# Kernel optimization log

Hardware: AMD Instinct MI355X
Metric: run time of the kernel (lower is better)

The kernel has to match this reference:

```python
import jax, jax.numpy as jnp
import numpy as np

LATENT, HID, STYLE, S = 16, 256, 64, 10
B = 16384

def _lin_init(key, fan_in, shape):
    # torch nn.Linear default: U(-1/sqrt(fan_in), 1/sqrt(fan_in))
    bound = 1.0 / np.sqrt(fan_in)
    return jax.random.uniform(key, shape, jnp.float32, -bound, bound)

def setup_inputs() -> dict:
    key = jax.random.key(0)
    ks = jax.random.split(key, 32)
    inp = {
        "z": jax.random.normal(ks[0], (B, LATENT), jnp.float32),
        "y": jax.random.randint(ks[1], (B,), 0, S),
        # shared 4-layer MLP
        "sw0": _lin_init(ks[2], LATENT, (LATENT, HID)), "sb0": _lin_init(ks[3], LATENT, (HID,)),
        "sw1": _lin_init(ks[4], HID, (HID, HID)), "sb1": _lin_init(ks[5], HID, (HID,)),
        "sw2": _lin_init(ks[6], HID, (HID, HID)), "sb2": _lin_init(ks[7], HID, (HID,)),
        "sw3": _lin_init(ks[8], HID, (HID, HID)), "sb3": _lin_init(ks[9], HID, (HID,)),
        # unshared per-speaker branches, stacked over speaker axis
        "uw0": _lin_init(ks[10], HID, (S, HID, HID)), "ub0": _lin_init(ks[11], HID, (S, HID)),
        "uw1": _lin_init(ks[12], HID, (S, HID, HID)), "ub1": _lin_init(ks[13], HID, (S, HID)),
        "uw2": _lin_init(ks[14], HID, (S, HID, HID)), "ub2": _lin_init(ks[15], HID, (S, HID)),
        "uw3": _lin_init(ks[16], HID, (S, HID, STYLE)), "ub3": _lin_init(ks[17], HID, (S, STYLE)),
    }
    return inp

def reference(z, y, sw0, sb0, sw1, sb1, sw2, sb2, sw3, sb3,
              uw0, ub0, uw1, ub1, uw2, ub2, uw3, ub3):
    relu = jax.nn.relu
    # shared trunk: [B, HID]
    h = relu(z @ sw0 + sb0)
    h = relu(h @ sw1 + sb1)
    h = relu(h @ sw2 + sb2)
    h = relu(h @ sw3 + sb3)
    # all speaker branches computed for every sample (faithful to original)
    t = relu(jnp.einsum('bh,shk->bsk', h, uw0) + ub0)  # [B, S, HID]
    t = relu(jnp.einsum('bsh,shk->bsk', t, uw1) + ub1)
    t = relu(jnp.einsum('bsh,shk->bsk', t, uw2) + ub2)
    out = jnp.einsum('bsh,shk->bsk', t, uw3) + ub3      # [B, S, STYLE]
    # gather branch by speaker id
    s = out[jnp.arange(out.shape[0]), y]                # [B, STYLE]
    return s
```

## Files before the change

### kernel.cpp

```cpp
#include <hip/hip_runtime.h>

#define B_TOT 16384
#define LAT   16
#define HID   256
#define STY   64
#define NS    10
#define RB    16
#define RB64  64
#define PAD   20
#define NBK   64

#define WS_CNT   0
#define WS_SEG   16
#define WS_BLK   32
#define WS_BCNT  64
#define WS_IDX   (WS_BCNT + NBK*NS)
#define IDX_CAP  (B_TOT + NS*RB64)
#define WS_INTS  (WS_IDX + IDX_CAP)
#define WGT_OFF_EL (((WS_INTS*4 + 255)/256)*128 + 384)
#define TOT_WEL  2334720
#define N_CHUNK  4560

typedef __attribute__((ext_vector_type(8))) short bf16x8;
typedef __attribute__((ext_vector_type(4))) float f32x4;

static __device__ __forceinline__ ushort f2bf(float x) {
    union { float f; unsigned u; } c; c.f = x;
    unsigned u = c.u;
    unsigned r = u + 0x7FFFu + ((u >> 16) & 1u);
    return (ushort)(r >> 16);
}

__global__ __launch_bounds__(256) void k_blkhist(const int* __restrict__ y, int* __restrict__ ws) {
    __shared__ int h[NS];
    int t = threadIdx.x;
    if (t < NS) h[t] = 0;
    __syncthreads();
    atomicAdd(&h[y[blockIdx.x * 256 + t]], 1);
    __syncthreads();
    if (t < NS) ws[WS_BCNT + blockIdx.x * NS + t] = h[t];
}

__global__ __launch_bounds__(256) void k_prep2(const int* __restrict__ y, int* __restrict__ ws, int rb) {
    __shared__ int tot_sh[NS], excl_sh[NS], off_sh[NS];
    const int t = threadIdx.x, wv = t >> 6, l = t & 63;
    const int myb = blockIdx.x;

    for (int s = wv; s < NS; s += 4) {
        int c = ws[WS_BCNT + l * NS + s];
        int inc = c;
        #pragma unroll
        for (int o = 1; o < 64; o <<= 1) {
            int v = __shfl_up(inc, o, 64);
            if (l >= o) inc += v;
        }
        int tot = __shfl(inc, 63, 64);
        int exc = __shfl(inc, myb, 64) - __shfl(c, myb, 64);
        if (l == 0) { tot_sh[s] = tot; excl_sh[s] = exc; }
    }
    __syncthreads();
    if (t < NS) {
        int ab = 0, ae = 0;
        for (int q = 0; q < t; ++q) {
            int cq = tot_sh[q];
            int nb = (cq + rb - 1) / rb;
            ab += nb; ae += nb * rb;
        }
        off_sh[t] = ae + excl_sh[t];
        if (myb == 0) {
            ws[WS_CNT + t] = tot_sh[t];
            ws[WS_SEG + t] = ae;
            ws[WS_BLK + t] = ab;
        }
    }
    if (myb == 0 && t == 0) {
        int ab = 0;
        for (int q = 0; q < NS; ++q) ab += (tot_sh[q] + rb - 1) / rb;
        ws[WS_BLK + NS] = ab;
    }
    __syncthreads();
    int b = myb * 256 + t;
    int p = atomicAdd(&off_sh[y[b]], 1);
    ws[WS_IDX + p] = b;
}

__global__ __launch_bounds__(256) void k_conv(
    const float* __restrict__ sw0, const float* __restrict__ sw1,
    const float* __restrict__ sw2, const float* __restrict__ sw3,
    const float* __restrict__ uw0, const float* __restrict__ uw1,
    const float* __restrict__ uw2, const float* __restrict__ uw3,
    ushort* __restrict__ wgt,
    const int* __restrict__ y, int* __restrict__ ws)
{
    __shared__ float tile[4][32][18];
    __shared__ int h[NS];

    if (blockIdx.x < NBK) {
        int t = threadIdx.x;
        if (t < NS) h[t] = 0;
        __syncthreads();
        atomicAdd(&h[y[blockIdx.x * 256 + t]], 1);
        __syncthreads();
        if (t < NS) ws[WS_BCNT + blockIdx.x * NS + t] = h[t];
    }

    int wid = blockIdx.x * 4 + (threadIdx.x >> 6);
    int wv  = threadIdx.x >> 6;
    int l   = threadIdx.x & 63;
    int lc  = l & 15, lh = l >> 4;

    const float* src; int Ksrc, N, kb, nt;
    if (wid < 16) {
        src = sw0; Ksrc = LAT; N = 256; kb = 0; nt = wid;
    } else if (wid < 400) {
        int c = wid - 16; int ly = c >> 7; int r = c & 127;
        src = (ly == 0 ? sw1 : ly == 1 ? sw2 : sw3);
        Ksrc = 256; N = 256; kb = r >> 4; nt = r & 15;
    } else {
        int c = wid - 400; int s = c / 416; int r = c % 416;
        if (r < 384) {
            int ly = r >> 7; int rr = r & 127;
            src = (ly == 0 ? uw0 : ly == 1 ? uw1 : uw2) + (long)s * 65536;
            Ksrc = 256; N = 256; kb = rr >> 4; nt = rr & 15;
        } else {
            int rr = r - 384;
            src = uw3 + (long)s * 16384;
            Ksrc = 256; N = STY; kb = rr >> 2; nt = rr & 3;
        }
    }

    #pragma unroll
    for (int it = 0; it < 2; ++it) {
        int r = it * 16 + (l >> 2);
        int k = kb * 32 + r;
        float4 v = make_float4(0.f, 0.f, 0.f, 0.f);
        if (k < Ksrc) v = *(const float4*)(src + (long)k * N + nt * 16 + (l & 3) * 4);
        int c = (l & 3) * 4;
        tile[wv][r][c] = v.x; tile[wv][r][c + 1] = v.y;
        tile[wv][r][c + 2] = v.z; tile[wv][r][c + 3] = v.w;
    }
    __syncthreads();

    ushort v[8];
    #pragma unroll
    for (int j = 0; j < 8; ++j) v[j] = f2bf(tile[wv][lh * 8 + j][lc]);
    uint4 o;
    o.x = (unsigned)v[0] | ((unsigned)v[1] << 16);
    o.y = (unsigned)v[2] | ((unsigned)v[3] << 16);
    o.z = (unsigned)v[4] | ((unsigned)v[5] << 16);
    o.w = (unsigned)v[6] | ((unsigned)v[7] << 16);
    *(uint4*)(wgt + (long)wid * 512 + l * 8) = o;
}

__global__ __launch_bounds__(512, 4) void k_main_bf(
    const float* __restrict__ z, const int* __restrict__ ws,
    const ushort* __restrict__ wgt,
    const float* __restrict__ sb0, const float* __restrict__ sb1,
    const float* __restrict__ sb2, const float* __restrict__ sb3,
    const float* __restrict__ ub0, const float* __restrict__ ub1,
    const float* __restrict__ ub2, const float* __restrict__ ub3,
    float* __restrict__ out)
{
    int bid = blockIdx.x;
    {
        int nwg = gridDim.x, q8 = nwg >> 3, r8 = nwg & 7;
        int x = bid & 7, p = bid >> 3;
        bid = (x < r8 ? x * (q8 + 1) : r8 * (q8 + 1) + (x - r8) * q8) + p;
    }
    if (bid >= ws[WS_BLK + NS]) return;

    int s = 0;
    #pragma unroll
    for (int q = 0; q < NS - 1; ++q)
        if (bid >= ws[WS_BLK + q + 1]) s = q + 1;
    const int loc  = bid - ws[WS_BLK + s];
    int nval = ws[WS_CNT + s] - loc * RB64;
    if (nval > RB64) nval = RB64;
    const int base = ws[WS_SEG + s] + loc * RB64;

    __shared__ ushort act[2][32][64][8];

    const int t = threadIdx.x, w = t >> 6, l = t & 63;
    const int lc = l & 15, lh = l >> 4;
    const int nt0 = w * 2;

    if (t < 256) {
        int row = t >> 2, q = t & 3;
        int gb  = ws[WS_IDX + base + row];
        if (row >= nval) gb = 0;
        float4 zv = *(const float4*)(z + (long)gb * LAT + q * 4);
        ushort4 pv; pv.x = f2bf(zv.x); pv.y = f2bf(zv.y); pv.z = f2bf(zv.z); pv.w = f2bf(zv.w);
        *(ushort4*)&act[0][q >> 1][row][(q & 1) * 4] = pv;
        ushort4 zr; zr.x = zr.y = zr.z = zr.w = 0;
        *(ushort4*)&act[0][2 + (q >> 1)][row][(q & 1) * 4] = zr;
    }
    __syncthreads();

    {
        f32x4 acc[2][4];
        #pragma unroll
        for (int q = 0; q < 2; ++q) {
            float4 bv = *(const float4*)(sb0 + (nt0 + q) * 16 + lh * 4);
            #pragma unroll
            for (int rt = 0; rt < 4; ++rt) acc[q][rt] = (f32x4){bv.x, bv.y, bv.z, bv.w};
        }
        bf16x8 Wf[2];
        #pragma unroll
        for (int q = 0; q < 2; ++q)
            Wf[q] = *(const bf16x8*)(wgt + ((nt0 + q) * 64 + l) * 8);
        #pragma unroll
        for (int rt = 0; rt < 4; ++rt) {
            bf16x8 av = *(const bf16x8*)&act[0][lh][rt * 16 + lc][0];
            #pragma unroll
            for (int q = 0; q < 2; ++q)
                acc[q][rt] = __builtin_amdgcn_mfma_f32_16x16x32_bf16(Wf[q], av, acc[q][rt], 0, 0, 0);
        }
        #pragma unroll
        for (int q = 0; q < 2; ++q) {
            int n0 = (nt0 + q) * 16 + lh * 4;
            #pragma unroll
            for (int rt = 0; rt < 4; ++rt) {
                ushort4 u;
                u.x = f2bf(fmaxf(acc[q][rt][0], 0.f));
                u.y = f2bf(fmaxf(acc[q][rt][1], 0.f));
                u.z = f2bf(fmaxf(acc[q][rt][2], 0.f));
                u.w = f2bf(fmaxf(acc[q][rt][3], 0.f));
                *(ushort4*)&act[1][n0 >> 3][rt * 16 + lc][n0 & 7] = u;
            }
        }
    }
    __syncthreads();

    auto midlayer = [&](const ushort* __restrict__ wf, const float* __restrict__ bs, int src) {
        const int dst = src ^ 1;
        f32x4 acc[2][4];
        #pragma unroll
        for (int q = 0; q < 2; ++q) {
            float4 bv = *(const float4*)(bs + (nt0 + q) * 16 + lh * 4);
            #pragma unroll
            for (int rt = 0; rt < 4; ++rt) acc[q][rt] = (f32x4){bv.x, bv.y, bv.z, bv.w};
        }
        bf16x8 Bc[2], Bn[2];
        #pragma unroll
        for (int q = 0; q < 2; ++q)
            Bc[q] = *(const bf16x8*)(wf + ((nt0 + q) * 64 + l) * 8);
        #pragma unroll
        for (int kb = 0; kb < 8; ++kb) {
            if (kb < 7) {
                #pragma unroll
                for (int q = 0; q < 2; ++q)
                    Bn[q] = *(const bf16x8*)(wf + (((kb + 1) * 16 + nt0 + q) * 64 + l) * 8);
            }
            #pragma unroll
            for (int rt = 0; rt < 4; ++rt) {
                bf16x8 av = *(const bf16x8*)&act[src][kb * 4 + lh][rt * 16 + lc][0];
                #pragma unroll
                for (int q = 0; q < 2; ++q)
                    acc[q][rt] = __builtin_amdgcn_mfma_f32_16x16x32_bf16(Bc[q], av, acc[q][rt], 0, 0, 0);
            }
            #pragma unroll
            for (int q = 0; q < 2; ++q) Bc[q] = Bn[q];
        }
        #pragma unroll
        for (int q = 0; q < 2; ++q) {
            int n0 = (nt0 + q) * 16 + lh * 4;
            #pragma unroll
            for (int rt = 0; rt < 4; ++rt) {
                ushort4 u;
                u.x = f2bf(fmaxf(acc[q][rt][0], 0.f));
                u.y = f2bf(fmaxf(acc[q][rt][1], 0.f));
                u.z = f2bf(fmaxf(acc[q][rt][2], 0.f));
                u.w = f2bf(fmaxf(acc[q][rt][3], 0.f));
                *(ushort4*)&act[dst][n0 >> 3][rt * 16 + lc][n0 & 7] = u;
            }
        }
        __syncthreads();
    };

    midlayer(wgt + 8192,   sb1, 1);
    midlayer(wgt + 73728,  sb2, 0);
    midlayer(wgt + 139264, sb3, 1);
    const long sbse = 204800 + (long)s * 212992;
    midlayer(wgt + sbse,          ub0 + s * HID, 0);
    midlayer(wgt + sbse + 65536,  ub1 + s * HID, 1);
    midlayer(wgt + sbse + 131072, ub2 + s * HID, 0);

    {
        const ushort* wf = wgt + sbse + 196608;
        const float*  bs = ub3 + s * STY;
        const int nt = w & 3, wr = w >> 2;
        const int n0 = nt * 16 + lh * 4;
        f32x4 acc[2];
        {
            float4 bv = *(const float4*)(bs + n0);
            acc[0] = (f32x4){bv.x, bv.y, bv.z, bv.w};
            acc[1] = acc[0];
        }
        bf16x8 Bc = *(const bf16x8*)(wf + (nt * 64 + l) * 8);
        bf16x8 Bn;
        #pragma unroll
        for (int kb = 0; kb < 8; ++kb) {
            if (kb < 7) Bn = *(const bf16x8*)(wf + (((kb + 1) * 4 + nt) * 64 + l) * 8);
            #pragma unroll
            for (int rtl = 0; rtl < 2; ++rtl) {
                int rt = wr * 2 + rtl;
                bf16x8 av = *(const bf16x8*)&act[1][kb * 4 + lh][rt * 16 + lc][0];
                acc[rtl] = __builtin_amdgcn_mfma_f32_16x16x32_bf16(Bc, av, acc[rtl], 0, 0, 0);
            }
            Bc = Bn;
        }
        #pragma unroll
        for (int rtl = 0; rtl < 2; ++rtl) {
            int row = (wr * 2 + rtl) * 16 + lc;
            if (row < nval) {
                int gb = ws[WS_IDX + base + row];
                float4 o = make_float4(acc[rtl][0], acc[rtl][1], acc[rtl][2], acc[rtl][3]);
                *(float4*)(out + (long)gb * STY + n0) = o;
            }
        }
    }
}

#define FMA16(wv_, hv_) do { \
    acc[0][0] = fmaf(hv_.x, wv_.x, acc[0][0]); \
    acc[0][1] = fmaf(hv_.y, wv_.x, acc[0][1]); \
    acc[0][2] = fmaf(hv_.z, wv_.x, acc[0][2]); \
    acc[0][3] = fmaf(hv_.w, wv_.x, acc[0][3]); \
    acc[1][0] = fmaf(hv_.x, wv_.y, acc[1][0]); \
    acc[1][1] = fmaf(hv_.y, wv_.y, acc[1][1]); \
    acc[1][2] = fmaf(hv_.z, wv_.y, acc[1][2]); \
    acc[1][3] = fmaf(hv_.w, wv_.y, acc[1][3]); \
    acc[2][0] = fmaf(hv_.x, wv_.z, acc[2][0]); \
    acc[2][1] = fmaf(hv_.y, wv_.z, acc[2][1]); \
    acc[2][2] = fmaf(hv_.z, wv_.z, acc[2][2]); \
    acc[2][3] = fmaf(hv_.w, wv_.z, acc[2][3]); \
    acc[3][0] = fmaf(hv_.x, wv_.w, acc[3][0]); \
    acc[3][1] = fmaf(hv_.y, wv_.w, acc[3][1]); \
    acc[3][2] = fmaf(hv_.z, wv_.w, acc[3][2]); \
    acc[3][3] = fmaf(hv_.w, wv_.w, acc[3][3]); \
} while (0)

__global__ __launch_bounds__(256, 3) void k_main_f32(
    const float* __restrict__ z,
    const int* __restrict__ ws,
    const float* __restrict__ sw0, const float* __restrict__ sb0,
    const float* __restrict__ sw1, const float* __restrict__ sb1,
    const float* __restrict__ sw2, const float* __restrict__ sb2,
    const float* __restrict__ sw3, const float* __restrict__ sb3,
    const float* __restrict__ uw0, const float* __restrict__ ub0,
    const float* __restrict__ uw1, const float* __restrict__ ub1,
    const float* __restrict__ uw2, const float* __restrict__ ub2,
    const float* __restrict__ uw3, const float* __restrict__ ub3,
    float* __restrict__ out)
{
    const int bid = blockIdx.x;
    if (bid >= ws[WS_BLK + NS]) return;
    int s = 0;
    #pragma unroll
    for (int q = 0; q < NS - 1; ++q)
        if (bid >= ws[WS_BLK + q + 1]) s = q + 1;
    const int loc  = bid - ws[WS_BLK + s];
    int nval = ws[WS_CNT + s] - loc * RB;
    if (nval > RB) nval = RB;
    const int base = ws[WS_SEG + s] + loc * RB;

    __shared__ int bidx[RB];
    __shared__ __align__(16) float zt[LAT][PAD];
    __shared__ __align__(16) float ht[2][HID][PAD];

    const int t = threadIdx.x;
    if (t < RB) {
        int gb = ws[WS_IDX + base + t];
        bidx[t] = (t < nval) ? gb : 0;
    }
    __syncthreads();
    { int r = t & (RB - 1), k = t >> 4; zt[k][r] = z[bidx[r] * LAT + k]; }
    __syncthreads();

    const int cg = t & 63, wvi = t >> 6, c0 = cg * 4, r0 = wvi * 4;
    float acc[4][4];
    {
        float4 bv = *(const float4*)(sb0 + c0);
        #pragma unroll
        for (int ri = 0; ri < 4; ++ri) { acc[0][ri] = bv.x; acc[1][ri] = bv.y; acc[2][ri] = bv.z; acc[3][ri] = bv.w; }
        #pragma unroll
        for (int k = 0; k < LAT; ++k) {
            float4 wv = *(const float4*)(sw0 + k * HID + c0);
            float4 hv = *(const float4*)(&zt[k][r0]);
            FMA16(wv, hv);
        }
        #pragma unroll
        for (int ci = 0; ci < 4; ++ci) {
            float4 v;
            v.x = fmaxf(acc[ci][0], 0.f); v.y = fmaxf(acc[ci][1], 0.f);
            v.z = fmaxf(acc[ci][2], 0.f); v.w = fmaxf(acc[ci][3], 0.f);
            *(float4*)&ht[0][c0 + ci][r0] = v;
        }
    }
    __syncthreads();

    auto midlayer = [&](const float* __restrict__ W, const float* __restrict__ bs, int src) {
        float4 bv = *(const float4*)(bs + c0);
        #pragma unroll
        for (int ri = 0; ri < 4; ++ri) { acc[0][ri] = bv.x; acc[1][ri] = bv.y; acc[2][ri] = bv.z; acc[3][ri] = bv.w; }
        #pragma unroll 4
        for (int k = 0; k < HID; ++k) {
            float4 wv = *(const float4*)(W + k * HID + c0);
            float4 hv = *(const float4*)(&ht[src][k][r0]);
            FMA16(wv, hv);
        }
        const int dst = src ^ 1;
        #pragma unroll
        for (int ci = 0; ci < 4; ++ci) {
            float4 v;
            v.x = fmaxf(acc[ci][0], 0.f); v.y = fmaxf(acc[ci][1], 0.f);
            v.z = fmaxf(acc[ci][2], 0.f); v.w = fmaxf(acc[ci][3], 0.f);
            *(float4*)&ht[dst][c0 + ci][r0] = v;
        }
    };

    midlayer(sw1, sb1, 0); __syncthreads();
    midlayer(sw2, sb2, 1); __syncthreads();
    midlayer(sw3, sb3, 0); __syncthreads();
    const long so = (long)s;
    midlayer(uw0 + so * HID * HID, ub0 + so * HID, 1); __syncthreads();
    midlayer(uw1 + so * HID * HID, ub1 + so * HID, 0); __syncthreads();
    midlayer(uw2 + so * HID * HID, ub2 + so * HID, 1); __syncthreads();

    {
        const float* W  = uw3 + so * HID * STY;
        const float* bs = ub3 + so * STY;
        const int c64 = (t & 15) * 4, rr = t >> 4;
        float4 bv = *(const float4*)(bs + c64);
        float a0 = bv.x, a1 = bv.y, a2 = bv.z, a3 = bv.w;
        #pragma unroll 4
        for (int k = 0; k < HID; ++k) {
            float4 wv = *(const float4*)(W + k * STY + c64);
            float  hv = ht[0][k][rr];
            a0 = fmaf(hv, wv.x, a0); a1 = fmaf(hv, wv.y, a1);
            a2 = fmaf(hv, wv.z, a2); a3 = fmaf(hv, wv.w, a3);
        }
        if (rr < nval) *(float4*)(out + (long)bidx[rr] * STY + c64) = make_float4(a0, a1, a2, a3);
    }
}

extern "C" void kernel_launch(void* const* d_in, const int* in_sizes, int n_in,
                              void* d_out, int out_size, void* d_ws, size_t ws_size,
                              hipStream_t stream) {
    const float* z   = (const float*)d_in[0];
    const int*   y   = (const int*)  d_in[1];
    const float* sw0 = (const float*)d_in[2];  const float* sb0 = (const float*)d_in[3];
    const float* sw1 = (const float*)d_in[4];  const float* sb1 = (const float*)d_in[5];
    const float* sw2 = (const float*)d_in[6];  const float* sb2 = (const float*)d_in[7];
    const float* sw3 = (const float*)d_in[8];  const float* sb3 = (const float*)d_in[9];
    const float* uw0 = (const float*)d_in[10]; const float* ub0 = (const float*)d_in[11];
    const float* uw1 = (const float*)d_in[12]; const float* ub1 = (const float*)d_in[13];
    const float* uw2 = (const float*)d_in[14]; const float* ub2 = (const float*)d_in[15];
    const float* uw3 = (const float*)d_in[16]; const float* ub3 = (const float*)d_in[17];
    float* out = (float*)d_out;
    int*   ws  = (int*)d_ws;

    const size_t req = (size_t)WGT_OFF_EL * 2 + (size_t)TOT_WEL * 2;
    const bool bfp = (ws_size >= req);

    if (bfp) {
        ushort* wgt = (ushort*)d_ws + WGT_OFF_EL;
        k_conv <<<N_CHUNK / 4, 256, 0, stream>>>(sw0, sw1, sw2, sw3, uw0, uw1, uw2, uw3, wgt, y, ws);
        k_prep2<<<NBK, 256, 0, stream>>>(y, ws, RB64);
        const int nblocks = B_TOT / RB64 + NS;
        k_main_bf<<<nblocks, 512, 0, stream>>>(z, ws, wgt,
            sb0, sb1, sb2, sb3, ub0, ub1, ub2, ub3, out);
    } else {
        k_blkhist<<<NBK, 256, 0, stream>>>(y, ws);
        k_prep2  <<<NBK, 256, 0, stream>>>(y, ws, RB);
        const int nblocks = B_TOT / RB + NS;
        k_main_f32<<<nblocks, 256, 0, stream>>>(z, ws,
            sw0, sb0, sw1, sb1, sw2, sb2, sw3, sb3,
            uw0, ub0, uw1, ub1, uw2, ub2, uw3, ub3, out);
    }
}
```

Before: 41.88 us.

## Fold speaker bucketing into main kernel, drop separate prep launch

Removes the k_prep2 launch and the histogram work in k_conv. Each main-kernel block now reads all of y, builds packed 16-bit per-speaker counts with a wave-level shuffle scan plus a cross-wave reduction, then works out its own speaker segment and fills a shared-memory index list. This cuts one kernel launch and the global workspace round-trip, at the cost of every block redundantly scanning the full 16K label array.

New measurement: 44.65 us. 6.6% more time.

```diff
diff --git a/kernel.cpp b/kernel.cpp
--- a/kernel.cpp
+++ b/kernel.cpp
@@ -17,7 +17,7 @@
 #define WS_IDX   (WS_BCNT + NBK*NS)
 #define IDX_CAP  (B_TOT + NS*RB64)
 #define WS_INTS  (WS_IDX + IDX_CAP)
-#define WGT_OFF_EL (((WS_INTS*4 + 255)/256)*128 + 384)
+#define WGT_OFF_EL (((WS_INTS*4 + 255)/256)*128)
 #define TOT_WEL  2334720
 #define N_CHUNK  4560
 
@@ -31,79 +31,14 @@
     return (ushort)(r >> 16);
 }
 
-__global__ __launch_bounds__(256) void k_blkhist(const int* __restrict__ y, int* __restrict__ ws) {
-    __shared__ int h[NS];
-    int t = threadIdx.x;
-    if (t < NS) h[t] = 0;
-    __syncthreads();
-    atomicAdd(&h[y[blockIdx.x * 256 + t]], 1);
-    __syncthreads();
-    if (t < NS) ws[WS_BCNT + blockIdx.x * NS + t] = h[t];
-}
-
-__global__ __launch_bounds__(256) void k_prep2(const int* __restrict__ y, int* __restrict__ ws, int rb) {
-    __shared__ int tot_sh[NS], excl_sh[NS], off_sh[NS];
-    const int t = threadIdx.x, wv = t >> 6, l = t & 63;
-    const int myb = blockIdx.x;
-
-    for (int s = wv; s < NS; s += 4) {
-        int c = ws[WS_BCNT + l * NS + s];
-        int inc = c;
-        #pragma unroll
-        for (int o = 1; o < 64; o <<= 1) {
-            int v = __shfl_up(inc, o, 64);
-            if (l >= o) inc += v;
-        }
-        int tot = __shfl(inc, 63, 64);
-        int exc = __shfl(inc, myb, 64) - __shfl(c, myb, 64);
-        if (l == 0) { tot_sh[s] = tot; excl_sh[s] = exc; }
-    }
-    __syncthreads();
-    if (t < NS) {
-        int ab = 0, ae = 0;
-        for (int q = 0; q < t; ++q) {
-            int cq = tot_sh[q];
-            int nb = (cq + rb - 1) / rb;
-            ab += nb; ae += nb * rb;
-        }
-        off_sh[t] = ae + excl_sh[t];
-        if (myb == 0) {
-            ws[WS_CNT + t] = tot_sh[t];
-            ws[WS_SEG + t] = ae;
-            ws[WS_BLK + t] = ab;
-        }
-    }
-    if (myb == 0 && t == 0) {
-        int ab = 0;
-        for (int q = 0; q < NS; ++q) ab += (tot_sh[q] + rb - 1) / rb;
-        ws[WS_BLK + NS] = ab;
-    }
-    __syncthreads();
-    int b = myb * 256 + t;
-    int p = atomicAdd(&off_sh[y[b]], 1);
-    ws[WS_IDX + p] = b;
-}
-
 __global__ __launch_bounds__(256) void k_conv(
     const float* __restrict__ sw0, const float* __restrict__ sw1,
     const float* __restrict__ sw2, const float* __restrict__ sw3,
     const float* __restrict__ uw0, const float* __restrict__ uw1,
     const float* __restrict__ uw2, const float* __restrict__ uw3,
-    ushort* __restrict__ wgt,
-    const int* __restrict__ y, int* __restrict__ ws)
+    ushort* __restrict__ wgt)
 {
     __shared__ float tile[4][32][18];
-    __shared__ int h[NS];
-
-    if (blockIdx.x < NBK) {
-        int t = threadIdx.x;
-        if (t < NS) h[t] = 0;
-        __syncthreads();
-        atomicAdd(&h[y[blockIdx.x * 256 + t]], 1);
-        __syncthreads();
-        if (t < NS) ws[WS_BCNT + blockIdx.x * NS + t] = h[t];
-    }
-
     int wid = blockIdx.x * 4 + (threadIdx.x >> 6);
     int wv  = threadIdx.x >> 6;
     int l   = threadIdx.x & 63;
@@ -153,7 +88,7 @@
 }
 
 __global__ __launch_bounds__(512, 4) void k_main_bf(
-    const float* __restrict__ z, const int* __restrict__ ws,
+    const float* __restrict__ z, const int* __restrict__ y,
     const ushort* __restrict__ wgt,
     const float* __restrict__ sb0, const float* __restrict__ sb1,
     const float* __restrict__ sb2, const float* __restrict__ sb3,
@@ -167,27 +102,86 @@
         int x = bid & 7, p = bid >> 3;
         bid = (x < r8 ? x * (q8 + 1) : r8 * (q8 + 1) + (x - r8) * q8) + p;
     }
-    if (bid >= ws[WS_BLK + NS]) return;
-
-    int s = 0;
-    #pragma unroll
-    for (int q = 0; q < NS - 1; ++q)
-        if (bid >= ws[WS_BLK + q + 1]) s = q + 1;
-    const int loc  = bid - ws[WS_BLK + s];
-    int nval = ws[WS_CNT + s] - loc * RB64;
-    if (nval > RB64) nval = RB64;
-    const int base = ws[WS_SEG + s] + loc * RB64;
 
     __shared__ ushort act[2][32][64][8];
+    __shared__ int bidx[RB64];
+    __shared__ unsigned long long wtot[8][3];
 
     const int t = threadIdx.x, w = t >> 6, l = t & 63;
     const int lc = l & 15, lh = l >> 4;
     const int nt0 = w * 2;
 
+    int4 yv[8];
+    {
+        const int4* yp = (const int4*)(y + t * 32);
+        #pragma unroll
+        for (int r = 0; r < 8; ++r) yv[r] = yp[r];
+    }
+    unsigned long long a0 = 0, a1 = 0, a2 = 0;
+    #define BUMP(v_) do { int v__ = (v_); \
+        if (v__ < 4)      a0 += 1ULL << (v__ * 16); \
+        else if (v__ < 8) a1 += 1ULL << ((v__ - 4) * 16); \
+        else              a2 += 1ULL << ((v__ - 8) * 16); } while (0)
+    #pragma unroll
+    for (int r = 0; r < 8; ++r) { BUMP(yv[r].x); BUMP(yv[r].y); BUMP(yv[r].z); BUMP(yv[r].w); }
+    #undef BUMP
+
+    unsigned long long s0 = a0, s1 = a1, s2 = a2;
+    #pragma unroll
+    for (int o = 1; o < 64; o <<= 1) {
+        unsigned long long v0 = __shfl_up(s0, o, 64);
+        unsigned long long v1 = __shfl_up(s1, o, 64);
+        unsigned long long v2 = __shfl_up(s2, o, 64);
+        if (l >= o) { s0 += v0; s1 += v1; s2 += v2; }
+    }
+    if (l == 63) { wtot[w][0] = s0; wtot[w][1] = s1; wtot[w][2] = s2; }
+    __syncthreads();
+    unsigned long long g0 = 0, g1 = 0, g2 = 0, we0 = 0, we1 = 0, we2 = 0;
+    #pragma unroll
+    for (int q = 0; q < 8; ++q) {
+        unsigned long long u0 = wtot[q][0], u1 = wtot[q][1], u2 = wtot[q][2];
+        if (q < w) { we0 += u0; we1 += u1; we2 += u2; }
+        g0 += u0; g1 += u1; g2 += u2;
+    }
+    unsigned long long p0 = we0 + s0 - a0, p1 = we1 + s1 - a1, p2 = we2 + s2 - a2;
+
+    #define TOTQ(q_) ((int)(((q_) < 4 ? g0 : ((q_) < 8 ? g1 : g2)) >> (((q_) & 3) * 16)) & 0xFFFF)
+    int s = -1, loc = 0, cnt = 0;
+    {
+        int ab = 0;
+        #pragma unroll
+        for (int q = 0; q < NS; ++q) {
+            int tq = TOTQ(q);
+            int nb = (tq + 63) >> 6;
+            if (s < 0 && bid < ab + nb) { s = q; loc = bid - ab; cnt = tq; }
+            ab += nb;
+        }
+    }
+    #undef TOTQ
+    if (s < 0) return;
+    int nval = cnt - loc * RB64;
+    if (nval > RB64) nval = RB64;
+
+    {
+        unsigned long long pw = (s < 4) ? p0 : ((s < 8) ? p1 : p2);
+        int rank = (int)((pw >> ((s & 3) * 16)) & 0xFFFF) - loc * RB64;
+        int gi = t * 32;
+        #pragma unroll
+        for (int r = 0; r < 8; ++r) {
+            int4 v = yv[r];
+            if (v.x == s) { if ((unsigned)rank < (unsigned)RB64) bidx[rank] = gi;     ++rank; }
+            if (v.y == s) { if ((unsigned)rank < (unsigned)RB64) bidx[rank] = gi + 1; ++rank; }
+            if (v.z == s) { if ((unsigned)rank < (unsigned)RB64) bidx[rank] = gi + 2; ++rank; }
+            if (v.w == s) { if ((unsigned)rank < (unsigned)RB64) bidx[rank] = gi + 3; ++rank; }
+            gi += 4;
+        }
+    }
+    __syncthreads();
+
     if (t < 256) {
         int row = t >> 2, q = t & 3;
-        int gb  = ws[WS_IDX + base + row];
-        if (row >= nval) gb = 0;
+        int gb  = (row < nval) ? bidx[row] : bidx[0];
+        if (nval <= 0) gb = 0;
         float4 zv = *(const float4*)(z + (long)gb * LAT + q * 4);
         ushort4 pv; pv.x = f2bf(zv.x); pv.y = f2bf(zv.y); pv.z = f2bf(zv.z); pv.w = f2bf(zv.w);
         *(ushort4*)&act[0][q >> 1][row][(q & 1) * 4] = pv;
@@ -313,12 +307,64 @@
         for (int rtl = 0; rtl < 2; ++rtl) {
             int row = (wr * 2 + rtl) * 16 + lc;
             if (row < nval) {
-                int gb = ws[WS_IDX + base + row];
+                int gb = bidx[row];
                 float4 o = make_float4(acc[rtl][0], acc[rtl][1], acc[rtl][2], acc[rtl][3]);
                 *(float4*)(out + (long)gb * STY + n0) = o;
             }
         }
     }
+}
+
+__global__ __launch_bounds__(256) void k_blkhist(const int* __restrict__ y, int* __restrict__ ws) {
+    __shared__ int h[NS];
+    int t = threadIdx.x;
+    if (t < NS) h[t] = 0;
+    __syncthreads();
+    atomicAdd(&h[y[blockIdx.x * 256 + t]], 1);
+    __syncthreads();
+    if (t < NS) ws[WS_BCNT + blockIdx.x * NS + t] = h[t];
+}
+
+__global__ __launch_bounds__(256) void k_prep2(const int* __restrict__ y, int* __restrict__ ws, int rb) {
+    __shared__ int tot_sh[NS], excl_sh[NS], off_sh[NS];
+    const int t = threadIdx.x, wv = t >> 6, l = t & 63;
+    const int myb = blockIdx.x;
+    for (int s = wv; s < NS; s += 4) {
+        int c = ws[WS_BCNT + l * NS + s];
+        int inc = c;
+        #pragma unroll
+        for (int o = 1; o < 64; o <<= 1) {
+            int v = __shfl_up(inc, o, 64);
+            if (l >= o) inc += v;
+        }
+        int tot = __shfl(inc, 63, 64);
+        int exc = __shfl(inc, myb, 64) - __shfl(c, myb, 64);
+        if (l == 0) { tot_sh[s] = tot; excl_sh[s] = exc; }
+    }
+    __syncthreads();
+    if (t < NS) {
+        int ab = 0, ae = 0;
+        for (int q = 0; q < t; ++q) {
+            int cq = tot_sh[q];
+            int nb = (cq + rb - 1) / rb;
+            ab += nb; ae += nb * rb;
+        }
+        off_sh[t] = ae + excl_sh[t];
+        if (myb == 0) {
+            ws[WS_CNT + t] = tot_sh[t];
+            ws[WS_SEG + t] = ae;
+            ws[WS_BLK + t] = ab;
+        }
+    }
+    if (myb == 0 && t == 0) {
+        int ab = 0;
+        for (int q = 0; q < NS; ++q) ab += (tot_sh[q] + rb - 1) / rb;
+        ws[WS_BLK + NS] = ab;
+    }
+    __syncthreads();
+    int b = myb * 256 + t;
+    int p = atomicAdd(&off_sh[y[b]], 1);
+    ws[WS_IDX + p] = b;
 }
 
 #define FMA16(wv_, hv_) do { \
@@ -465,10 +511,9 @@
 
     if (bfp) {
         ushort* wgt = (ushort*)d_ws + WGT_OFF_EL;
-        k_conv <<<N_CHUNK / 4, 256, 0, stream>>>(sw0, sw1, sw2, sw3, uw0, uw1, uw2, uw3, wgt, y, ws);
-        k_prep2<<<NBK, 256, 0, stream>>>(y, ws, RB64);
+        k_conv<<<N_CHUNK / 4, 256, 0, stream>>>(sw0, sw1, sw2, sw3, uw0, uw1, uw2, uw3, wgt);
         const int nblocks = B_TOT / RB64 + NS;
-        k_main_bf<<<nblocks, 512, 0, stream>>>(z, ws, wgt,
+        k_main_bf<<<nblocks, 512, 0, stream>>>(z, y, wgt,
             sb0, sb1, sb2, sb3, ub0, ub1, ub2, ub3, out);
     } else {
         k_blkhist<<<NBK, 256, 0, stream>>>(y, ws);
```

## Fold speaker bucketing into conversion kernel and deepen weight prefetch to three stages

Applied to the files above, without the earlier changes.

Removes the separate k_prep2 launch by having block 0 of the weight-conversion kernel compute the speaker histogram, prefix sums and the sorted index list on its own. It uses packed 16-bit counters in 64-bit words and wave scans for this. This cuts one kernel launch and the per-block histogram round trip through global memory, at the cost of serialising the bucketing onto a single block. The MFMA layers also switch from double-buffered to triple-buffered B-fragment prefetch, so global weight loads get more latency hiding at the cost of extra registers.

Result: slower. 46.14 us (+10.2%).

```diff
diff --git a/kernel.cpp b/kernel.cpp
--- a/kernel.cpp
+++ b/kernel.cpp
@@ -17,12 +17,13 @@
 #define WS_IDX   (WS_BCNT + NBK*NS)
 #define IDX_CAP  (B_TOT + NS*RB64)
 #define WS_INTS  (WS_IDX + IDX_CAP)
-#define WGT_OFF_EL (((WS_INTS*4 + 255)/256)*128 + 384)
+#define WGT_OFF_EL (((WS_INTS*4 + 255)/256)*128)
 #define TOT_WEL  2334720
 #define N_CHUNK  4560
 
 typedef __attribute__((ext_vector_type(8))) short bf16x8;
 typedef __attribute__((ext_vector_type(4))) float f32x4;
+typedef unsigned long long ull;
 
 static __device__ __forceinline__ ushort f2bf(float x) {
     union { float f; unsigned u; } c; c.f = x;
@@ -31,60 +32,7 @@
     return (ushort)(r >> 16);
 }
 
-__global__ __launch_bounds__(256) void k_blkhist(const int* __restrict__ y, int* __restrict__ ws) {
-    __shared__ int h[NS];
-    int t = threadIdx.x;
-    if (t < NS) h[t] = 0;
-    __syncthreads();
-    atomicAdd(&h[y[blockIdx.x * 256 + t]], 1);
-    __syncthreads();
-    if (t < NS) ws[WS_BCNT + blockIdx.x * NS + t] = h[t];
-}
-
-__global__ __launch_bounds__(256) void k_prep2(const int* __restrict__ y, int* __restrict__ ws, int rb) {
-    __shared__ int tot_sh[NS], excl_sh[NS], off_sh[NS];
-    const int t = threadIdx.x, wv = t >> 6, l = t & 63;
-    const int myb = blockIdx.x;
-
-    for (int s = wv; s < NS; s += 4) {
-        int c = ws[WS_BCNT + l * NS + s];
-        int inc = c;
-        #pragma unroll
-        for (int o = 1; o < 64; o <<= 1) {
-            int v = __shfl_up(inc, o, 64);
-            if (l >= o) inc += v;
-        }
-        int tot = __shfl(inc, 63, 64);
-        int exc = __shfl(inc, myb, 64) - __shfl(c, myb, 64);
-        if (l == 0) { tot_sh[s] = tot; excl_sh[s] = exc; }
-    }
-    __syncthreads();
-    if (t < NS) {
-        int ab = 0, ae = 0;
-        for (int q = 0; q < t; ++q) {
-            int cq = tot_sh[q];
-            int nb = (cq + rb - 1) / rb;
-            ab += nb; ae += nb * rb;
-        }
-        off_sh[t] = ae + excl_sh[t];
-        if (myb == 0) {
-            ws[WS_CNT + t] = tot_sh[t];
-            ws[WS_SEG + t] = ae;
-            ws[WS_BLK + t] = ab;
-        }
-    }
-    if (myb == 0 && t == 0) {
-        int ab = 0;
-        for (int q = 0; q < NS; ++q) ab += (tot_sh[q] + rb - 1) / rb;
-        ws[WS_BLK + NS] = ab;
-    }
-    __syncthreads();
-    int b = myb * 256 + t;
-    int p = atomicAdd(&off_sh[y[b]], 1);
-    ws[WS_IDX + p] = b;
-}
-
-__global__ __launch_bounds__(256) void k_conv(
+__global__ __launch_bounds__(256) void k_pre(
     const float* __restrict__ sw0, const float* __restrict__ sw1,
     const float* __restrict__ sw2, const float* __restrict__ sw3,
     const float* __restrict__ uw0, const float* __restrict__ uw1,
@@ -92,19 +40,90 @@
     ushort* __restrict__ wgt,
     const int* __restrict__ y, int* __restrict__ ws)
 {
+    if (blockIdx.x == 0) {
+        const int t = threadIdx.x, w = t >> 6, l = t & 63;
+        __shared__ ull wtot[4][3];
+        int4 yv[16];
+        const int4* yp = (const int4*)(y + t * 64);
+        #pragma unroll
+        for (int r = 0; r < 16; ++r) yv[r] = yp[r];
+
+        ull a0 = 0, a1 = 0, a2 = 0;
+        #define BUMP(v_) do { int v__ = (v_); \
+            if (v__ < 4)      a0 += 1ULL << (v__ * 16); \
+            else if (v__ < 8) a1 += 1ULL << ((v__ - 4) * 16); \
+            else              a2 += 1ULL << ((v__ - 8) * 16); } while (0)
+        #pragma unroll
+        for (int r = 0; r < 16; ++r) { BUMP(yv[r].x); BUMP(yv[r].y); BUMP(yv[r].z); BUMP(yv[r].w); }
+        #undef BUMP
+
+        ull s0 = a0, s1 = a1, s2 = a2;
+        #pragma unroll
+        for (int o = 1; o < 64; o <<= 1) {
+            ull v0 = __shfl_up(s0, o, 64);
+            ull v1 = __shfl_up(s1, o, 64);
+            ull v2 = __shfl_up(s2, o, 64);
+            if (l >= o) { s0 += v0; s1 += v1; s2 += v2; }
+        }
+        if (l == 63) { wtot[w][0] = s0; wtot[w][1] = s1; wtot[w][2] = s2; }
+        __syncthreads();
+        ull g0 = 0, g1 = 0, g2 = 0, we0 = 0, we1 = 0, we2 = 0;
+        #pragma unroll
+        for (int q = 0; q < 4; ++q) {
+            ull u0 = wtot[q][0], u1 = wtot[q][1], u2 = wtot[q][2];
+            if (q < w) { we0 += u0; we1 += u1; we2 += u2; }
+            g0 += u0; g1 += u1; g2 += u2;
+        }
+        ull q0 = we0 + s0 - a0, q1 = we1 + s1 - a1, q2 = we2 + s2 - a2;
+
+        #define TOTQ(q_) ((int)(((q_) < 4 ? g0 : ((q_) < 8 ? g1 : g2)) >> (((q_) & 3) * 16)) & 0xFFFF)
+        ull sg0 = 0, sg1 = 0, sg2 = 0;
+        {
+            int ae = 0;
+            #pragma unroll
+            for (int q = 0; q < NS; ++q) {
+                if (q < 4)      sg0 |= (ull)ae << (q * 16);
+                else if (q < 8) sg1 |= (ull)ae << ((q - 4) * 16);
+                else            sg2 |= (ull)ae << ((q - 8) * 16);
+                ae += ((TOTQ(q) + RB64 - 1) >> 6) << 6;
+            }
+        }
+        if (t < NS) {
+            int ab = 0, ae = 0;
+            for (int q = 0; q < t; ++q) {
+                int tq = TOTQ(q);
+                int nb = (tq + RB64 - 1) >> 6;
+                ab += nb; ae += nb << 6;
+            }
+            ws[WS_CNT + t] = TOTQ(t);
+            ws[WS_SEG + t] = ae;
+            ws[WS_BLK + t] = ab;
+        }
+        if (t == 0) {
+            int ab = 0;
+            #pragma unroll
+            for (int q = 0; q < NS; ++q) ab += (TOTQ(q) + RB64 - 1) >> 6;
+            ws[WS_BLK + NS] = ab;
+        }
+        #undef TOTQ
+        int gi = t * 64;
+        #pragma unroll
+        for (int r = 0; r < 16; ++r) {
+            int vv[4] = { yv[r].x, yv[r].y, yv[r].z, yv[r].w };
+            #pragma unroll
+            for (int c = 0; c < 4; ++c) {
+                int v = vv[c], sh = (v & 3) * 16, dst;
+                if (v < 4)      { dst = (int)(((sg0 + q0) >> sh) & 0xFFFF); q0 += 1ULL << sh; }
+                else if (v < 8) { dst = (int)(((sg1 + q1) >> sh) & 0xFFFF); q1 += 1ULL << sh; }
+                else            { dst = (int)(((sg2 + q2) >> sh) & 0xFFFF); q2 += 1ULL << sh; }
+                ws[WS_IDX + dst] = gi + r * 4 + c;
+            }
+        }
+        return;
+    }
+
     __shared__ float tile[4][32][18];
-    __shared__ int h[NS];
-
-    if (blockIdx.x < NBK) {
-        int t = threadIdx.x;
-        if (t < NS) h[t] = 0;
-        __syncthreads();
-        atomicAdd(&h[y[blockIdx.x * 256 + t]], 1);
-        __syncthreads();
-        if (t < NS) ws[WS_BCNT + blockIdx.x * NS + t] = h[t];
-    }
-
-    int wid = blockIdx.x * 4 + (threadIdx.x >> 6);
+    int wid = (blockIdx.x - 1) * 4 + (threadIdx.x >> 6);
     int wv  = threadIdx.x >> 6;
     int l   = threadIdx.x & 63;
     int lc  = l & 15, lh = l >> 4;
@@ -240,26 +259,27 @@
             #pragma unroll
             for (int rt = 0; rt < 4; ++rt) acc[q][rt] = (f32x4){bv.x, bv.y, bv.z, bv.w};
         }
-        bf16x8 Bc[2], Bn[2];
-        #pragma unroll
-        for (int q = 0; q < 2; ++q)
-            Bc[q] = *(const bf16x8*)(wf + ((nt0 + q) * 64 + l) * 8);
+        bf16x8 Bq[3][2];
+        #pragma unroll
+        for (int d = 0; d < 3; ++d)
+            #pragma unroll
+            for (int q = 0; q < 2; ++q)
+                Bq[d][q] = *(const bf16x8*)(wf + ((d * 16 + nt0 + q) * 64 + l) * 8);
         #pragma unroll
         for (int kb = 0; kb < 8; ++kb) {
-            if (kb < 7) {
-                #pragma unroll
-                for (int q = 0; q < 2; ++q)
-                    Bn[q] = *(const bf16x8*)(wf + (((kb + 1) * 16 + nt0 + q) * 64 + l) * 8);
-            }
+            const int d = kb % 3;
             #pragma unroll
             for (int rt = 0; rt < 4; ++rt) {
                 bf16x8 av = *(const bf16x8*)&act[src][kb * 4 + lh][rt * 16 + lc][0];
                 #pragma unroll
                 for (int q = 0; q < 2; ++q)
-                    acc[q][rt] = __builtin_amdgcn_mfma_f32_16x16x32_bf16(Bc[q], av, acc[q][rt], 0, 0, 0);
-            }
-            #pragma unroll
-            for (int q = 0; q < 2; ++q) Bc[q] = Bn[q];
+                    acc[q][rt] = __builtin_amdgcn_mfma_f32_16x16x32_bf16(Bq[d][q], av, acc[q][rt], 0, 0, 0);
+            }
+            if (kb + 3 < 8) {
+                #pragma unroll
+                for (int q = 0; q < 2; ++q)
+                    Bq[d][q] = *(const bf16x8*)(wf + (((kb + 3) * 16 + nt0 + q) * 64 + l) * 8);
+            }
         }
         #pragma unroll
         for (int q = 0; q < 2; ++q) {
@@ -296,18 +316,20 @@
             acc[0] = (f32x4){bv.x, bv.y, bv.z, bv.w};
             acc[1] = acc[0];
         }
-        bf16x8 Bc = *(const bf16x8*)(wf + (nt * 64 + l) * 8);
-        bf16x8 Bn;
+        bf16x8 Bq[3];
+        #pragma unroll
+        for (int d = 0; d < 3; ++d)
+            Bq[d] = *(const bf16x8*)(wf + ((d * 4 + nt) * 64 + l) * 8);
         #pragma unroll
         for (int kb = 0; kb < 8; ++kb) {
-            if (kb < 7) Bn = *(const bf16x8*)(wf + (((kb + 1) * 4 + nt) * 64 + l) * 8);
+            const int d = kb % 3;
             #pragma unroll
             for (int rtl = 0; rtl < 2; ++rtl) {
                 int rt = wr * 2 + rtl;
                 bf16x8 av = *(const bf16x8*)&act[1][kb * 4 + lh][rt * 16 + lc][0];
-                acc[rtl] = __builtin_amdgcn_mfma_f32_16x16x32_bf16(Bc, av, acc[rtl], 0, 0, 0);
-            }
-            Bc = Bn;
+                acc[rtl] = __builtin_amdgcn_mfma_f32_16x16x32_bf16(Bq[d], av, acc[rtl], 0, 0, 0);
+            }
+            if (kb + 3 < 8) Bq[d] = *(const bf16x8*)(wf + (((kb + 3) * 4 + nt) * 64 + l) * 8);
         }
         #pragma unroll
         for (int rtl = 0; rtl < 2; ++rtl) {
@@ -319,6 +341,58 @@
             }
         }
     }
+}
+
+__global__ __launch_bounds__(256) void k_blkhist(const int* __restrict__ y, int* __restrict__ ws) {
+    __shared__ int h[NS];
+    int t = threadIdx.x;
+    if (t < NS) h[t] = 0;
+    __syncthreads();
+    atomicAdd(&h[y[blockIdx.x * 256 + t]], 1);
+    __syncthreads();
+    if (t < NS) ws[WS_BCNT + blockIdx.x * NS + t] = h[t];
+}
+
+__global__ __launch_bounds__(256) void k_prep2(const int* __restrict__ y, int* __restrict__ ws, int rb) {
+    __shared__ int tot_sh[NS], excl_sh[NS], off_sh[NS];
+    const int t = threadIdx.x, wv = t >> 6, l = t & 63;
+    const int myb = blockIdx.x;
+    for (int s = wv; s < NS; s += 4) {
+        int c = ws[WS_BCNT + l * NS + s];
+        int inc = c;
+        #pragma unroll
+        for (int o = 1; o < 64; o <<= 1) {
+            int v = __shfl_up(inc, o, 64);
+            if (l >= o) inc += v;
+        }
+        int tot = __shfl(inc, 63, 64);
+        int exc = __shfl(inc, myb, 64) - __shfl(c, myb, 64);
+        if (l == 0) { tot_sh[s] = tot; excl_sh[s] = exc; }
+    }
+    __syncthreads();
+    if (t < NS) {
+        int ab = 0, ae = 0;
+        for (int q = 0; q < t; ++q) {
+            int cq = tot_sh[q];
+            int nb = (cq + rb - 1) / rb;
+            ab += nb; ae += nb * rb;
+        }
+        off_sh[t] = ae + excl_sh[t];
+        if (myb == 0) {
+            ws[WS_CNT + t] = tot_sh[t];
+            ws[WS_SEG + t] = ae;
+            ws[WS_BLK + t] = ab;
+        }
+    }
+    if (myb == 0 && t == 0) {
+        int ab = 0;
+        for (int q = 0; q < NS; ++q) ab += (tot_sh[q] + rb - 1) / rb;
+        ws[WS_BLK + NS] = ab;
+    }
+    __syncthreads();
+    int b = myb * 256 + t;
+    int p = atomicAdd(&off_sh[y[b]], 1);
+    ws[WS_IDX + p] = b;
 }
 
 #define FMA16(wv_, hv_) do { \
@@ -465,8 +539,7 @@
 
     if (bfp) {
         ushort* wgt = (ushort*)d_ws + WGT_OFF_EL;
-        k_conv <<<N_CHUNK / 4, 256, 0, stream>>>(sw0, sw1, sw2, sw3, uw0, uw1, uw2, uw3, wgt, y, ws);
-        k_prep2<<<NBK, 256, 0, stream>>>(y, ws, RB64);
+        k_pre<<<N_CHUNK / 4 + 1, 256, 0, stream>>>(sw0, sw1, sw2, sw3, uw0, uw1, uw2, uw3, wgt, y, ws);
         const int nblocks = B_TOT / RB64 + NS;
         k_main_bf<<<nblocks, 512, 0, stream>>>(z, ws, wgt,
             sb0, sb1, sb2, sb3, ub0, ub1, ub2, ub3, out);
```

## Fuse speaker-bucketing scan into main kernel, drop separate prep launch

Applied to the files above, without the earlier changes.

Removes the k_prep2 launch. Each main-kernel block now runs a wavefront prefix scan over the per-chunk speaker histograms, which k_conv appears to produce. It then finds its speaker segment and builds its own 64-row index list in shared memory by scanning the relevant chunks of y. This saves one kernel launch and the global index-array round trip. In exchange, every block redoes the histogram scan and reads parts of y, which adds shared memory and sync overhead at the start of each block.

New measurement: 40.87 us. 1.02x faster.

```diff
diff --git a/kernel.cpp b/kernel.cpp
--- a/kernel.cpp
+++ b/kernel.cpp
@@ -23,6 +23,7 @@
 
 typedef __attribute__((ext_vector_type(8))) short bf16x8;
 typedef __attribute__((ext_vector_type(4))) float f32x4;
+typedef unsigned long long ull;
 
 static __device__ __forceinline__ ushort f2bf(float x) {
     union { float f; unsigned u; } c; c.f = x;
@@ -153,8 +154,8 @@
 }
 
 __global__ __launch_bounds__(512, 4) void k_main_bf(
-    const float* __restrict__ z, const int* __restrict__ ws,
-    const ushort* __restrict__ wgt,
+    const float* __restrict__ z, const int* __restrict__ y,
+    const int* __restrict__ ws, const ushort* __restrict__ wgt,
     const float* __restrict__ sb0, const float* __restrict__ sb1,
     const float* __restrict__ sb2, const float* __restrict__ sb3,
     const float* __restrict__ ub0, const float* __restrict__ ub1,
@@ -167,27 +168,83 @@
         int x = bid & 7, p = bid >> 3;
         bid = (x < r8 ? x * (q8 + 1) : r8 * (q8 + 1) + (x - r8) * q8) + p;
     }
-    if (bid >= ws[WS_BLK + NS]) return;
-
-    int s = 0;
-    #pragma unroll
-    for (int q = 0; q < NS - 1; ++q)
-        if (bid >= ws[WS_BLK + q + 1]) s = q + 1;
-    const int loc  = bid - ws[WS_BLK + s];
-    int nval = ws[WS_CNT + s] - loc * RB64;
-    if (nval > RB64) nval = RB64;
-    const int base = ws[WS_SEG + s] + loc * RB64;
 
     __shared__ ushort act[2][32][64][8];
+    __shared__ ull pk[65][3];
+    __shared__ int bidx[RB64];
 
     const int t = threadIdx.x, w = t >> 6, l = t & 63;
     const int lc = l & 15, lh = l >> 4;
     const int nt0 = w * 2;
 
+    if (w == 0) {
+        const int* cb = ws + WS_BCNT + l * NS;
+        ull a0 = (ull)cb[0] | ((ull)cb[1] << 16) | ((ull)cb[2] << 32) | ((ull)cb[3] << 48);
+        ull a1 = (ull)cb[4] | ((ull)cb[5] << 16) | ((ull)cb[6] << 32) | ((ull)cb[7] << 48);
+        ull a2 = (ull)cb[8] | ((ull)cb[9] << 16);
+        ull s0 = a0, s1 = a1, s2 = a2;
+        #pragma unroll
+        for (int o = 1; o < 64; o <<= 1) {
+            ull v0 = __shfl_up(s0, o, 64);
+            ull v1 = __shfl_up(s1, o, 64);
+            ull v2 = __shfl_up(s2, o, 64);
+            if (l >= o) { s0 += v0; s1 += v1; s2 += v2; }
+        }
+        pk[l][0] = s0 - a0; pk[l][1] = s1 - a1; pk[l][2] = s2 - a2;
+        if (l == 63) { pk[64][0] = s0; pk[64][1] = s1; pk[64][2] = s2; }
+    }
+    __syncthreads();
+
+    const ull g0 = pk[64][0], g1 = pk[64][1], g2 = pk[64][2];
+    #define TOTQ(q_) ((int)((((q_) < 4) ? g0 : (((q_) < 8) ? g1 : g2)) >> (((q_) & 3) * 16)) & 0xFFFF)
+    int s = -1, loc = 0, cnt = 0;
+    {
+        int ab = 0;
+        #pragma unroll
+        for (int q = 0; q < NS; ++q) {
+            int tq = TOTQ(q);
+            int nb = (tq + 63) >> 6;
+            if (s < 0 && bid < ab + nb) { s = q; loc = bid - ab; cnt = tq; }
+            ab += nb;
+        }
+    }
+    #undef TOTQ
+    if (s < 0) return;
+    int nval = cnt - loc * RB64;
+    if (nval > RB64) nval = RB64;
+    const int lo = loc * RB64, hi = lo + RB64;
+    const int sh = (s & 3) * 16;
+
+    #pragma unroll
+    for (int bo = 0; bo < 8; ++bo) {
+        int b = w * 8 + bo;
+        ull pbp = (s < 4) ? pk[b][0]     : ((s < 8) ? pk[b][1]     : pk[b][2]);
+        ull pnp = (s < 4) ? pk[b + 1][0] : ((s < 8) ? pk[b + 1][1] : pk[b + 1][2]);
+        int Pb = (int)((pbp >> sh) & 0xFFFF);
+        int Pn = (int)((pnp >> sh) & 0xFFFF);
+        if (Pb < hi && Pn > lo) {
+            int4 v = *(const int4*)(y + b * 256 + l * 4);
+            int m0 = (v.x == s), m1 = (v.y == s), m2 = (v.z == s), m3 = (v.w == s);
+            int c = m0 + m1 + m2 + m3;
+            int inc = c;
+            #pragma unroll
+            for (int o = 1; o < 64; o <<= 1) {
+                int u = __shfl_up(inc, o, 64);
+                if (l >= o) inc += u;
+            }
+            int r  = Pb + inc - c;
+            int gi = b * 256 + l * 4;
+            if (m0) { if (r >= lo && r < hi) bidx[r - lo] = gi;     ++r; }
+            if (m1) { if (r >= lo && r < hi) bidx[r - lo] = gi + 1; ++r; }
+            if (m2) { if (r >= lo && r < hi) bidx[r - lo] = gi + 2; ++r; }
+            if (m3) { if (r >= lo && r < hi) bidx[r - lo] = gi + 3; ++r; }
+        }
+    }
+    __syncthreads();
+
     if (t < 256) {
         int row = t >> 2, q = t & 3;
-        int gb  = ws[WS_IDX + base + row];
-        if (row >= nval) gb = 0;
+        int gb  = (row < nval) ? bidx[row] : 0;
         float4 zv = *(const float4*)(z + (long)gb * LAT + q * 4);
         ushort4 pv; pv.x = f2bf(zv.x); pv.y = f2bf(zv.y); pv.z = f2bf(zv.z); pv.w = f2bf(zv.w);
         *(ushort4*)&act[0][q >> 1][row][(q & 1) * 4] = pv;
@@ -313,7 +370,7 @@
         for (int rtl = 0; rtl < 2; ++rtl) {
             int row = (wr * 2 + rtl) * 16 + lc;
             if (row < nval) {
-                int gb = ws[WS_IDX + base + row];
+                int gb = bidx[row];
                 float4 o = make_float4(acc[rtl][0], acc[rtl][1], acc[rtl][2], acc[rtl][3]);
                 *(float4*)(out + (long)gb * STY + n0) = o;
             }
@@ -465,10 +522,9 @@
 
     if (bfp) {
         ushort* wgt = (ushort*)d_ws + WGT_OFF_EL;
-        k_conv <<<N_CHUNK / 4, 256, 0, stream>>>(sw0, sw1, sw2, sw3, uw0, uw1, uw2, uw3, wgt, y, ws);
-        k_prep2<<<NBK, 256, 0, stream>>>(y, ws, RB64);
+        k_conv<<<N_CHUNK / 4, 256, 0, stream>>>(sw0, sw1, sw2, sw3, uw0, uw1, uw2, uw3, wgt, y, ws);
         const int nblocks = B_TOT / RB64 + NS;
-        k_main_bf<<<nblocks, 512, 0, stream>>>(z, ws, wgt,
+        k_main_bf<<<nblocks, 512, 0, stream>>>(z, y, ws, wgt,
             sb0, sb1, sb2, sb3, ub0, ub1, ub2, ub3, out);
     } else {
         k_blkhist<<<NBK, 256, 0, stream>>>(y, ws);
```
